# Performance work log

Hardware: AMD Instinct MI355X
Metric: run time of the kernel (lower is better)

## Reference

```python
import jax, jax.numpy as jnp
import numpy as np

# Architecture constants (from RUMamba.__init__ hard-coded Mamba2 config)
D_MODEL = 512
D_STATE = 128
D_CONV = 4
EXPAND = 4
HEADDIM = 32
D_INNER = EXPAND * D_MODEL            # 2048
NHEADS = D_INNER // HEADDIM           # 64
CONV_DIM = D_INNER + 2 * D_STATE      # 2304 (ngroups=1)
D_IN_PROJ = 2 * D_INNER + 2 * D_STATE + NHEADS  # 4416
NUM_CLASS = 2513
BATCH = 4
SEQ = 16


def setup_inputs() -> dict:
    key = jax.random.key(0)
    ks = jax.random.split(key, 8)
    inputs = jax.random.normal(ks[0], (BATCH, SEQ, D_MODEL), jnp.float32)
    in_proj_w = jax.random.normal(ks[1], (D_IN_PROJ, D_MODEL), jnp.float32) * 0.02
    conv_w = jax.random.normal(ks[2], (CONV_DIM, D_CONV), jnp.float32) * 0.2
    conv_b = jnp.zeros((CONV_DIM,), jnp.float32)
    # dt_bias initialized so softplus(dt_bias) ~ U(0.001, 0.1), as in Mamba2
    dt = jax.random.uniform(ks[3], (NHEADS,), jnp.float32, 0.001, 0.1)
    dt_bias = dt + jnp.log(-jnp.expm1(-dt))
    A_log = jnp.log(jax.random.uniform(ks[4], (NHEADS,), jnp.float32, 1.0, 16.0))
    cls_w = jax.random.normal(ks[5], (NUM_CLASS, HEADDIM * D_STATE), jnp.float32) * 0.02
    cls_b = jnp.zeros((NUM_CLASS,), jnp.float32)
    return {"inputs": inputs, "in_proj_w": in_proj_w, "conv_w": conv_w,
            "conv_b": conv_b, "dt_bias": dt_bias, "A_log": A_log,
            "cls_w": cls_w, "cls_b": cls_b}


def reference(inputs, in_proj_w, conv_w, conv_b, dt_bias, A_log, cls_w, cls_b):
    # inputs: (B, S, D) -> (S, B, D) as in forward's permute(1,0,2)
    seq = jnp.transpose(inputs, (1, 0, 2))
    S, B, _ = seq.shape

    # Shared in_proj for both rolling and unrolling (same Mamba math on inputs[t]).
    zxbcdt = jnp.einsum('sbd,ed->sbe', seq, in_proj_w)        # (S,B,4416)
    xBC_raw = zxbcdt[..., D_INNER:D_INNER + CONV_DIM]          # (S,B,2304)
    dt = jax.nn.softplus(zxbcdt[..., -NHEADS:] + dt_bias)      # (S,B,H)
    A = -jnp.exp(A_log)                                        # (H,)
    dA = jnp.exp(dt * A)                                       # (S,B,H)

    # --- Rolling pass: one length-1 Mamba call per timestep, SSM state carried,
    # conv state NOT carried -> causal conv on a length-1 seq uses only last tap.
    xBC_r = jax.nn.silu(xBC_raw * conv_w[:, -1] + conv_b)      # (S,B,2304)
    x_r = xBC_r[..., :D_INNER].reshape(S, B, NHEADS, HEADDIM)  # (S,B,H,P)
    B_r = xBC_r[..., D_INNER:D_INNER + D_STATE]                # (S,B,N)
    dBx = dt[..., None, None] * B_r[:, :, None, None, :] * x_r[..., None]  # (S,B,H,P,N)

    def roll_step(h, inp):
        dA_t, dBx_t = inp
        h = dA_t[..., None, None] * h + dBx_t
        return h, h

    h0 = jnp.zeros((B, NHEADS, HEADDIM, D_STATE), seq.dtype)
    _, states = jax.lax.scan(roll_step, h0, (dA, dBx))         # (S,B,H,P,N)

    # --- Unrolling pass: for each t, feed inputs[t] repeated (S - t + 1) times
    # starting from states[t]. Constant input => conv output only depends on
    # min(step, d_conv-1) via cumulative sums of reversed conv taps.
    cw = jnp.cumsum(conv_w[:, ::-1], axis=1)                   # (2304,4)
    t_idx = jnp.arange(S)

    def unroll_step(h, k):
        w_k = cw[:, jnp.minimum(k, D_CONV - 1)]                # (2304,)
        xBC_k = jax.nn.silu(xBC_raw * w_k + conv_b)            # (S,B,2304)
        x_k = xBC_k[..., :D_INNER].reshape(S, B, NHEADS, HEADDIM)
        B_k = xBC_k[..., D_INNER:D_INNER + D_STATE]
        h_new = dA[..., None, None] * h + \
            dt[..., None, None] * B_k[:, :, None, None, :] * x_k[..., None]
        active = (k <= S - t_idx)[:, None, None, None, None]   # length S - t + 1
        return jnp.where(active, h_new, h), None

    h_fin, _ = jax.lax.scan(unroll_step, states, jnp.arange(S + 1))  # (S,B,H,P,N)

    # Head-reduce to headdim*d_state = 4096 features, classify.
    feats = jnp.mean(h_fin, axis=2).reshape(S, B, HEADDIM * D_STATE)
    feats = jnp.transpose(feats, (1, 0, 2))                    # (B,S,4096)
    y = feats @ cls_w.T + cls_b                                # (B,S,num_class)
    return y
```

## Files before the change

kernel.cpp:

```cpp
#include <hip/hip_runtime.h>
#include <math.h>

#define S_LEN    16
#define NTOK     64
#define DMODEL   512
#define XB_COLS  2176
#define ZX_COLS  2240
#define NCLASS   2513
#define FEATDIM  4096
#define PD_STRIDE 2516
#define APAD     68

typedef float f4v __attribute__((ext_vector_type(4)));

__global__ __launch_bounds__(256) void k_fpart(const float* __restrict__ X,
                                               const float* __restrict__ W,
                                               float* __restrict__ partF) {
    const int tid = threadIdx.x;
    const int kf  = blockIdx.y;
    const int jb  = blockIdx.x * 64;
    const int k0  = kf * 64;

    __shared__ float A[64][64];
    __shared__ float B[64][64];

    {
        const int t  = tid >> 2;
        const int kq = tid & 3;
        const int xrow = (t & 3) * 16 + (t >> 2);
        const int e = (jb + t < XB_COLS) ? (2048 + jb + t) : (2176 + jb + t);
#pragma unroll
        for (int q = 0; q < 4; ++q) {
            const int kk = kq * 16 + q * 4;
            const float4 va = *reinterpret_cast<const float4*>(
                X + (size_t)xrow * DMODEL + k0 + kk);
            A[kk + 0][t] = va.x; A[kk + 1][t] = va.y;
            A[kk + 2][t] = va.z; A[kk + 3][t] = va.w;
            const float4 vb = *reinterpret_cast<const float4*>(
                W + (size_t)e * DMODEL + k0 + kk);
            B[kk + 0][t] = vb.x; B[kk + 1][t] = vb.y;
            B[kk + 2][t] = vb.z; B[kk + 3][t] = vb.w;
        }
    }
    __syncthreads();

    const int ti = tid >> 4;
    const int ci = tid & 15;
    float acc[4][4] = {{0.f}};
#pragma unroll 4
    for (int k = 0; k < 64; ++k) {
        const f4v a = *reinterpret_cast<const f4v*>(&A[k][ti * 4]);
        const f4v b = *reinterpret_cast<const f4v*>(&B[k][ci * 4]);
#pragma unroll
        for (int j = 0; j < 4; ++j)
#pragma unroll
            for (int l = 0; l < 4; ++l)
                acc[j][l] += a[j] * b[l];
    }
#pragma unroll
    for (int jj = 0; jj < 4; ++jj) {
        f4v s; s[0] = acc[jj][0]; s[1] = acc[jj][1];
               s[2] = acc[jj][2]; s[3] = acc[jj][3];
        *reinterpret_cast<f4v*>(
            partF + ((size_t)kf * NTOK + ti * 4 + jj) * ZX_COLS + jb + ci * 4) = s;
    }
}

__global__ __launch_bounds__(256) void k_fepi(const float* __restrict__ partF, int KF,
                                              const float* __restrict__ conv_w,
                                              const float* __restrict__ conv_b,
                                              const float* __restrict__ dt_bias,
                                              const float* __restrict__ A_log,
                                              float* __restrict__ u,
                                              float* __restrict__ aArr,
                                              float* __restrict__ dArr) {
    const int idx4 = blockIdx.x * 256 + threadIdx.x;
    const int m  = idx4 / 560;
    const int j  = (idx4 - m * 560) * 4;

    f4v acc = {0.f, 0.f, 0.f, 0.f};
    for (int kf = 0; kf < KF; ++kf)
        acc += *reinterpret_cast<const f4v*>(
            partF + ((size_t)kf * NTOK + m) * ZX_COLS + j);

    if (j < XB_COLS) {
        float wk[4][4], cb[4];
#pragma unroll
        for (int e = 0; e < 4; ++e) {
            const float4 cwv = *reinterpret_cast<const float4*>(conv_w + (j + e) * 4);
            cb[e] = conv_b[j + e];
            wk[e][0] = cwv.w;
            wk[e][1] = wk[e][0] + cwv.z;
            wk[e][2] = wk[e][1] + cwv.y;
            wk[e][3] = wk[e][2] + cwv.x;
        }
#pragma unroll
        for (int k = 0; k < 4; ++k) {
            f4v o;
#pragma unroll
            for (int e = 0; e < 4; ++e) {
                const float v = acc[e] * wk[e][k] + cb[e];
                o[e] = v / (1.f + expf(-v));
            }
            *reinterpret_cast<f4v*>(u + ((size_t)k * NTOK + m) * XB_COLS + j) = o;
        }
    } else {
        const int h = j - XB_COLS;
        f4v dv, av;
#pragma unroll
        for (int e = 0; e < 4; ++e) {
            const float x = acc[e] + dt_bias[h + e];
            const float d = (x > 20.f) ? x : log1pf(expf(x));
            dv[e] = d;
            av[e] = expf(-d * expf(A_log[h + e]));
        }
        *reinterpret_cast<f4v*>(dArr + m * 64 + h) = dv;
        *reinterpret_cast<f4v*>(aArr + m * 64 + h) = av;
    }
}

__global__ __launch_bounds__(256) void k_feats(const float* __restrict__ u,
                                               const float* __restrict__ aArr,
                                               const float* __restrict__ dArr,
                                               float* __restrict__ feats) {
    const int bx = blockIdx.x;
    const int g  = bx & 3;
    const int tb = bx >> 2;
    const int t  = tb >> 2;
    const int b  = tb & 3;
    const int tid = threadIdx.x;
    const int K = 16 - t;
    const int nvec = t + 5;

    __shared__ float q[16][64];
    __shared__ float cu[4][64];
    __shared__ float WV[20][8];
    __shared__ float Bv[20][128];

    if (tid < 64) {
        const int h = tid;
        const int mt = t * 4 + b;
        const float a   = aArr[mt * 64 + h];
        const float dtv = dArr[mt * 64 + h];
        float p = 1.f;
        float c3 = 0.f, c2 = 0.f, c1 = 0.f, c0 = 0.f, cs = 0.f;
        for (int j = 0; j <= K + 1; ++j) {
            if (j <= K - 3) c3 += p;
            if (j == K - 2) c2 = p;
            if (j == K - 1) c1 = p;
            if (j == K)     c0 = p;
            if (j == K + 1) cs = p;
            p *= a;
        }
        cu[0][h] = dtv * c0;
        cu[1][h] = dtv * c1;
        cu[2][h] = dtv * c2;
        cu[3][h] = dtv * c3;
        float prod = 1.f;
        for (int s = t; s >= 0; --s) {
            const int ms = s * 4 + b;
            q[s][h] = cs * prod * dArr[ms * 64 + h];
            prod *= aArr[ms * 64 + h];
        }
    }
    __syncthreads();

    {
        const int il = tid & 7;
        const int i  = g * 8 + il;
        const int vs = tid >> 3;
        for (int v = vs; v < nvec; v += 32) {
            float acc = 0.f;
            if (v <= t) {
                const float* base = u + (size_t)(v * 4 + b) * XB_COLS;
                for (int h = 0; h < 64; ++h) acc += q[v][h] * base[h * 32 + i];
            } else {
                const int kk = v - t - 1;
                const float* base = u + ((size_t)kk * NTOK + t * 4 + b) * XB_COLS;
                for (int h = 0; h < 64; ++h) acc += cu[kk][h] * base[h * 32 + i];
            }
            WV[v][il] = acc;
        }
    }
    for (int x = tid; x < nvec * 128; x += 256) {
        const int v = x >> 7, n = x & 127;
        size_t src;
        if (v <= t) src = (size_t)(v * 4 + b) * XB_COLS + 2048 + n;
        else        src = ((size_t)(v - t - 1) * NTOK + t * 4 + b) * XB_COLS + 2048 + n;
        Bv[v][n] = u[src];
    }
    __syncthreads();

    {
        const int il = tid >> 5;
        const int i  = g * 8 + il;
        const int n0 = (tid & 31) * 4;
        const int r  = b * 16 + t;
        float acc[4] = {0.f, 0.f, 0.f, 0.f};
        for (int v = 0; v < nvec; ++v) {
            const float wvv = WV[v][il];
#pragma unroll
            for (int nn = 0; nn < 4; ++nn) acc[nn] += wvv * Bv[v][n0 + nn];
        }
        f4v o;
#pragma unroll
        for (int nn = 0; nn < 4; ++nn) o[nn] = acc[nn] * (1.f / 64.f);
        *reinterpret_cast<f4v*>(feats + (size_t)r * FEATDIM + i * 128 + n0) = o;
    }
}

__global__ __launch_bounds__(256) void k_cls(const float* __restrict__ feats,
                                             const float* __restrict__ Wc,
                                             float* __restrict__ partialD) {
    const int tid   = threadIdx.x;
    const int lane  = tid & 63;
    const int wv    = tid >> 6;
    const int ks    = blockIdx.y;
    const int cls0  = blockIdx.x * 64;
    const int chunk = FEATDIM / gridDim.y;
    const int nsub  = chunk / 64;

    __shared__ float lds[12288];
    float* A = lds;
    float* B = lds + 64 * APAD;

    const int rq = tid >> 4;
    const int kq = tid & 15;
    int crow[4];
#pragma unroll
    for (int r = 0; r < 4; ++r) {
        int cr = cls0 + rq * 4 + r; if (cr > NCLASS - 1) cr = NCLASS - 1;
        crow[r] = cr;
    }

    const int ti = lane >> 3;
    const int ci = lane & 7;

    float4 pa[4], pb[4];
#define LOADREGS(ST)                                                      \
    do {                                                                  \
        const int k0_ = ks * chunk + (ST) * 64 + kq * 4;                  \
        _Pragma("unroll")                                                 \
        for (int r = 0; r < 4; ++r) {                                     \
            pa[r] = *reinterpret_cast<const float4*>(                     \
                feats + (size_t)(rq * 4 + r) * FEATDIM + k0_);            \
            pb[r] = *reinterpret_cast<const float4*>(                     \
                Wc + (size_t)crow[r] * FEATDIM + k0_);                    \
        }                                                                 \
    } while (0)

    float acc[8][8] = {{0.f}};

    LOADREGS(0);
    for (int st = 0; st < nsub; ++st) {
        __syncthreads();
        {
#pragma unroll
            for (int s = 0; s < 4; ++s) {
                const int kk = kq * 4 + s;
                f4v wa; wa[0] = (&pa[0].x)[s]; wa[1] = (&pa[1].x)[s];
                        wa[2] = (&pa[2].x)[s]; wa[3] = (&pa[3].x)[s];
                *reinterpret_cast<f4v*>(&A[kk * APAD + rq * 4]) = wa;
                f4v wb; wb[0] = (&pb[0].x)[s]; wb[1] = (&pb[1].x)[s];
                        wb[2] = (&pb[2].x)[s]; wb[3] = (&pb[3].x)[s];
                *reinterpret_cast<f4v*>(&B[kk * APAD + rq * 4]) = wb;
            }
        }
        if (st + 1 < nsub) LOADREGS(st + 1);
        __syncthreads();

#pragma unroll
        for (int k = 0; k < 16; ++k) {
            const int kk = wv * 16 + k;
            const f4v a0 = *reinterpret_cast<const f4v*>(&A[kk * APAD + ti * 4]);
            const f4v a1 = *reinterpret_cast<const f4v*>(&A[kk * APAD + 32 + ti * 4]);
            const f4v b0 = *reinterpret_cast<const f4v*>(&B[kk * APAD + ci * 4]);
            const f4v b1 = *reinterpret_cast<const f4v*>(&B[kk * APAD + 32 + ci * 4]);
#pragma unroll
            for (int j = 0; j < 4; ++j) {
#pragma unroll
                for (int l = 0; l < 4; ++l) {
                    acc[j][l]         += a0[j] * b0[l];
                    acc[j][l + 4]     += a0[j] * b1[l];
                    acc[j + 4][l]     += a1[j] * b0[l];
                    acc[j + 4][l + 4] += a1[j] * b1[l];
                }
            }
        }
    }
#undef LOADREGS

    const size_t obase = (size_t)ks * (NTOK * PD_STRIDE);
#pragma unroll
    for (int half = 0; half < 2; ++half) {
        __syncthreads();
#pragma unroll
        for (int i = 0; i < 32; ++i)
            lds[wv * 2048 + i * 64 + lane] = acc[half * 4 + (i >> 3)][i & 7];
        __syncthreads();

        float s[8];
#pragma unroll
        for (int l = 0; l < 8; ++l)
            s[l] = lds[          (wv * 8 + l) * 64 + lane]
                 + lds[2048 +    (wv * 8 + l) * 64 + lane]
                 + lds[4096 +    (wv * 8 + l) * 64 + lane]
                 + lds[6144 +    (wv * 8 + l) * 64 + lane];

        const int row = half * 32 + ti * 4 + wv;
#pragma unroll
        for (int cb = 0; cb < 2; ++cb) {
            const int c = cls0 + cb * 32 + ci * 4;
            f4v v4;
#pragma unroll
            for (int l = 0; l < 4; ++l) v4[l] = s[cb * 4 + l];
            float* dst = partialD + obase + (size_t)row * PD_STRIDE + c;
            if (c + 3 < NCLASS) {
                *reinterpret_cast<f4v*>(dst) = v4;
            } else {
#pragma unroll
                for (int l = 0; l < 4; ++l)
                    if (c + l < NCLASS) dst[l] = v4[l];
            }
        }
    }
}

__global__ void k_out(const float* __restrict__ partialD, const float* __restrict__ cls_b,
                      float* __restrict__ out, int NP) {
    const int bx = blockIdx.x;
    const int r  = bx / 10;
    const int c  = (bx % 10) * 256 + threadIdx.x;
    if (c >= NCLASS) return;
    float s = cls_b[c];
    for (int p = 0; p < NP; ++p)
        s += partialD[(size_t)p * (NTOK * PD_STRIDE) + (size_t)r * PD_STRIDE + c];
    out[(size_t)r * NCLASS + c] = s;
}

extern "C" void kernel_launch(void* const* d_in, const int* in_sizes, int n_in,
                              void* d_out, int out_size, void* d_ws, size_t ws_size,
                              hipStream_t stream) {
    const float* inputs  = (const float*)d_in[0];
    const float* in_proj = (const float*)d_in[1];
    const float* conv_w  = (const float*)d_in[2];
    const float* conv_b  = (const float*)d_in[3];
    const float* dt_bias = (const float*)d_in[4];
    const float* A_log   = (const float*)d_in[5];
    const float* cls_w   = (const float*)d_in[6];
    const float* cls_b   = (const float*)d_in[7];
    float* out = (float*)d_out;

    float* ws = (float*)d_ws;
    float* aArr    = ws;
    float* dArr    = ws + 4096;
    float* feats   = ws + 8192;
    float* scr     = ws + 270336;
    float* u       = scr;
    float* partF   = scr + 557056;
    float* partialD = scr;

    int KC;
    if (ws_size >= 11386880u) KC = 16;
    else                      KC = 8;

    k_fpart <<<dim3(35, 8), 256, 0, stream>>>(inputs, in_proj, partF);
    k_fepi  <<<140, 256, 0, stream>>>(partF, 8, conv_w, conv_b, dt_bias, A_log,
                                      u, aArr, dArr);
    k_feats <<<256, 256, 0, stream>>>(u, aArr, dArr, feats);
    k_cls   <<<dim3(40, KC), 256, 0, stream>>>(feats, cls_w, partialD);
    k_out   <<<640, 256, 0, stream>>>(partialD, cls_b, out, KC);
}
```

Baseline: 60.23 us.

## Fuse five kernels into one persistent kernel with global barriers

Merges the five separate launches (projection GEMM, epilogue, state/features, classifier GEMM, reduction) into a single persistent kernel of 256 blocks. The phases are separated by atomic-counter grid barriers in workspace memory, which is zeroed with a memset before the launch. This removes per-launch overhead and the gaps between kernels. In exchange, phases with more work units than blocks are serialized within each block, and correctness relies on all 256 blocks being co-resident, with no cooperative-launch guarantee.

```diff
diff --git a/kernel.cpp b/kernel.cpp
--- a/kernel.cpp
+++ b/kernel.cpp
@@ -13,17 +13,29 @@
 
 typedef float f4v __attribute__((ext_vector_type(4)));
 
-__global__ __launch_bounds__(256) void k_fpart(const float* __restrict__ X,
-                                               const float* __restrict__ W,
-                                               float* __restrict__ partF) {
-    const int tid = threadIdx.x;
-    const int kf  = blockIdx.y;
-    const int jb  = blockIdx.x * 64;
-    const int k0  = kf * 64;
-
-    __shared__ float A[64][64];
-    __shared__ float B[64][64];
-
+__device__ __forceinline__ void gsync(unsigned* bar, int idx) {
+    __syncthreads();
+    if (threadIdx.x == 0) {
+        __threadfence();
+        atomicAdd(&bar[idx], 1u);
+        while (atomicAdd(&bar[idx], 0u) < 256u)
+            __builtin_amdgcn_s_sleep(8);
+        __threadfence();
+    }
+    __syncthreads();
+}
+
+__device__ __forceinline__ void phaseA(float* lds, int unit, int tid,
+                                       const float* __restrict__ X,
+                                       const float* __restrict__ W,
+                                       float* __restrict__ partF) {
+    const int kf = unit / 35;
+    const int jb = (unit % 35) * 64;
+    const int k0 = kf * 64;
+    float (*A)[64] = (float(*)[64])lds;
+    float (*B)[64] = (float(*)[64])(lds + 4096);
+
+    __syncthreads();
     {
         const int t  = tid >> 2;
         const int kq = tid & 3;
@@ -66,15 +78,16 @@
     }
 }
 
-__global__ __launch_bounds__(256) void k_fepi(const float* __restrict__ partF, int KF,
-                                              const float* __restrict__ conv_w,
-                                              const float* __restrict__ conv_b,
-                                              const float* __restrict__ dt_bias,
-                                              const float* __restrict__ A_log,
-                                              float* __restrict__ u,
-                                              float* __restrict__ aArr,
-                                              float* __restrict__ dArr) {
-    const int idx4 = blockIdx.x * 256 + threadIdx.x;
+__device__ __forceinline__ void phaseB(int unit, int tid,
+                                       const float* __restrict__ partF, int KF,
+                                       const float* __restrict__ conv_w,
+                                       const float* __restrict__ conv_b,
+                                       const float* __restrict__ dt_bias,
+                                       const float* __restrict__ A_log,
+                                       float* __restrict__ u,
+                                       float* __restrict__ aArr,
+                                       float* __restrict__ dArr) {
+    const int idx4 = unit * 256 + tid;
     const int m  = idx4 / 560;
     const int j  = (idx4 - m * 560) * 4;
 
@@ -119,24 +132,24 @@
     }
 }
 
-__global__ __launch_bounds__(256) void k_feats(const float* __restrict__ u,
-                                               const float* __restrict__ aArr,
-                                               const float* __restrict__ dArr,
-                                               float* __restrict__ feats) {
-    const int bx = blockIdx.x;
+__device__ __forceinline__ void phaseC(float* lds, int bx, int tid,
+                                       const float* __restrict__ u,
+                                       const float* __restrict__ aArr,
+                                       const float* __restrict__ dArr,
+                                       float* __restrict__ feats) {
     const int g  = bx & 3;
     const int tb = bx >> 2;
     const int t  = tb >> 2;
     const int b  = tb & 3;
-    const int tid = threadIdx.x;
     const int K = 16 - t;
     const int nvec = t + 5;
 
-    __shared__ float q[16][64];
-    __shared__ float cu[4][64];
-    __shared__ float WV[20][8];
-    __shared__ float Bv[20][128];
-
+    float (*q)[64]   = (float(*)[64])lds;
+    float (*cu)[64]  = (float(*)[64])(lds + 1024);
+    float (*WV)[8]   = (float(*)[8])(lds + 1280);
+    float (*Bv)[128] = (float(*)[128])(lds + 1440);
+
+    __syncthreads();
     if (tid < 64) {
         const int h = tid;
         const int mt = t * 4 + b;
@@ -207,20 +220,20 @@
         for (int nn = 0; nn < 4; ++nn) o[nn] = acc[nn] * (1.f / 64.f);
         *reinterpret_cast<f4v*>(feats + (size_t)r * FEATDIM + i * 128 + n0) = o;
     }
-}
-
-__global__ __launch_bounds__(256) void k_cls(const float* __restrict__ feats,
-                                             const float* __restrict__ Wc,
-                                             float* __restrict__ partialD) {
-    const int tid   = threadIdx.x;
+    __syncthreads();
+}
+
+__device__ __forceinline__ void phaseD(float* lds, int unit, int tid, int KC,
+                                       const float* __restrict__ feats,
+                                       const float* __restrict__ Wc,
+                                       float* __restrict__ partialD) {
     const int lane  = tid & 63;
     const int wv    = tid >> 6;
-    const int ks    = blockIdx.y;
-    const int cls0  = blockIdx.x * 64;
-    const int chunk = FEATDIM / gridDim.y;
+    const int ks    = unit / 40;
+    const int cls0  = (unit % 40) * 64;
+    const int chunk = FEATDIM / KC;
     const int nsub  = chunk / 64;
 
-    __shared__ float lds[12288];
     float* A = lds;
     float* B = lds + 64 * APAD;
 
@@ -302,10 +315,10 @@
         float s[8];
 #pragma unroll
         for (int l = 0; l < 8; ++l)
-            s[l] = lds[          (wv * 8 + l) * 64 + lane]
-                 + lds[2048 +    (wv * 8 + l) * 64 + lane]
-                 + lds[4096 +    (wv * 8 + l) * 64 + lane]
-                 + lds[6144 +    (wv * 8 + l) * 64 + lane];
+            s[l] = lds[       (wv * 8 + l) * 64 + lane]
+                 + lds[2048 + (wv * 8 + l) * 64 + lane]
+                 + lds[4096 + (wv * 8 + l) * 64 + lane]
+                 + lds[6144 + (wv * 8 + l) * 64 + lane];
 
         const int row = half * 32 + ti * 4 + wv;
 #pragma unroll
@@ -324,18 +337,60 @@
             }
         }
     }
-}
-
-__global__ void k_out(const float* __restrict__ partialD, const float* __restrict__ cls_b,
-                      float* __restrict__ out, int NP) {
-    const int bx = blockIdx.x;
-    const int r  = bx / 10;
-    const int c  = (bx % 10) * 256 + threadIdx.x;
+    __syncthreads();
+}
+
+__device__ __forceinline__ void phaseE(int unit, int tid, int NP,
+                                       const float* __restrict__ partialD,
+                                       const float* __restrict__ cls_b,
+                                       float* __restrict__ out) {
+    const int r = unit / 10;
+    const int c = (unit % 10) * 256 + tid;
     if (c >= NCLASS) return;
     float s = cls_b[c];
     for (int p = 0; p < NP; ++p)
         s += partialD[(size_t)p * (NTOK * PD_STRIDE) + (size_t)r * PD_STRIDE + c];
     out[(size_t)r * NCLASS + c] = s;
+}
+
+__global__ __launch_bounds__(256) void k_mega(const float* __restrict__ X,
+                                              const float* __restrict__ W,
+                                              const float* __restrict__ conv_w,
+                                              const float* __restrict__ conv_b,
+                                              const float* __restrict__ dt_bias,
+                                              const float* __restrict__ A_log,
+                                              const float* __restrict__ Wc,
+                                              const float* __restrict__ cls_b,
+                                              float* __restrict__ partF,
+                                              float* __restrict__ u,
+                                              float* __restrict__ aArr,
+                                              float* __restrict__ dArr,
+                                              float* __restrict__ feats,
+                                              float* __restrict__ partialD,
+                                              float* __restrict__ out,
+                                              unsigned* __restrict__ bar,
+                                              int KC) {
+    __shared__ float lds[12288];
+    const int bid = blockIdx.x;
+    const int tid = threadIdx.x;
+
+    for (int unit = bid; unit < 280; unit += 256)
+        phaseA(lds, unit, tid, X, W, partF);
+    gsync(bar, 0);
+
+    for (int unit = bid; unit < 140; unit += 256)
+        phaseB(unit, tid, partF, 8, conv_w, conv_b, dt_bias, A_log, u, aArr, dArr);
+    gsync(bar, 1);
+
+    phaseC(lds, bid, tid, u, aArr, dArr, feats);
+    gsync(bar, 2);
+
+    for (int unit = bid; unit < 40 * KC; unit += 256)
+        phaseD(lds, unit, tid, KC, feats, Wc, partialD);
+    gsync(bar, 3);
+
+    for (int unit = bid; unit < 640; unit += 256)
+        phaseE(unit, tid, KC, partialD, cls_b, out);
 }
 
 extern "C" void kernel_launch(void* const* d_in, const int* in_sizes, int n_in,
@@ -361,13 +416,14 @@
     float* partialD = scr;
 
     int KC;
-    if (ws_size >= 11386880u) KC = 16;
-    else                      KC = 8;
-
-    k_fpart <<<dim3(35, 8), 256, 0, stream>>>(inputs, in_proj, partF);
-    k_fepi  <<<140, 256, 0, stream>>>(partF, 8, conv_w, conv_b, dt_bias, A_log,
-                                      u, aArr, dArr);
-    k_feats <<<256, 256, 0, stream>>>(u, aArr, dArr, feats);
-    k_cls   <<<dim3(40, KC), 256, 0, stream>>>(feats, cls_w, partialD);
-    k_out   <<<640, 256, 0, stream>>>(partialD, cls_b, out, KC);
-}
+    size_t barOff;
+    if (ws_size >= 11386944u) { KC = 16; barOff = 270336 + 2576384; }
+    else                      { KC = 8;  barOff = 270336 + 1703936; }
+    unsigned* bar = (unsigned*)(ws + barOff);
+
+    hipMemsetAsync(bar, 0, 4 * sizeof(unsigned), stream);
+    k_mega<<<256, 256, 0, stream>>>(inputs, in_proj, conv_w, conv_b,
+                                    dt_bias, A_log, cls_w, cls_b,
+                                    partF, u, aArr, dArr, feats, partialD,
+                                    out, bar, KC);
+}
```

Result: slower. 167.4 us (+177.9%).
